# Optimization experiments

Hardware: AMD Instinct MI355X
Metric: run time of the kernel (lower is better)

The kernel has to match this reference:

```python
import jax, jax.numpy as jnp
import numpy as np
import math

N, KZ, IFZ, AHZ, AFZ = 2048, 20, 128, 4, 32
LN_EPS = 1e-5


def setup_inputs() -> dict:
    key = jax.random.key(0)
    ks = jax.random.split(key, 8)
    s = 1.0 / math.sqrt(IFZ)
    return {
        "x_2": jax.random.normal(ks[0], (N, KZ, IFZ), jnp.float32),
        "edge_index": jax.random.randint(ks[1], (N, KZ), 0, N, dtype=jnp.int64),
        "Wq": jax.random.normal(ks[2], (IFZ, AHZ * AFZ), jnp.float32) * s,
        "Wk": jax.random.normal(ks[3], (IFZ, AHZ * AFZ), jnp.float32) * s,
        "Wv": jax.random.normal(ks[4], (IFZ, AHZ * AFZ), jnp.float32) * s,
        "Wb": jax.random.normal(ks[5], (IFZ, AHZ), jnp.float32) * s,
        "Wg": jax.random.normal(ks[6], (IFZ, AHZ * AFZ), jnp.float32) * s,
        "bg": jnp.zeros((AHZ * AFZ,), jnp.float32),
        "Wback": jax.random.normal(ks[7], (AHZ * AFZ, IFZ), jnp.float32) * s,
        "bback": jnp.zeros((IFZ,), jnp.float32),
        "gamma": jnp.ones((IFZ,), jnp.float32),
        "beta": jnp.zeros((IFZ,), jnp.float32),
    }


def _edge_attention(x_2, edge_index, Wq, Wk, Wv, Wb, Wg, bg, Wback, bback, gamma, beta):
    n, kz, _ = x_2.shape
    ahz, afz = AHZ, AFZ
    # projections: [N, kz, ahz, afz]
    q = (x_2 @ Wq).reshape(n, kz, ahz, afz)
    k = (x_2 @ Wk).reshape(n, kz, ahz, afz)
    v = (x_2 @ Wv).reshape(n, kz, ahz, afz)
    gate = jax.nn.sigmoid((x_2 @ Wg + bg).reshape(n, kz, ahz, afz))
    b = x_2 @ Wb  # [N, kz, ahz]
    scale = math.sqrt(afz)
    # neighbor gathers: [N, kz, kz, ahz, afz] (dominant memory traffic)
    k_nb = k[edge_index]
    v_nb = v[edge_index]
    b_nb = b[edge_index]  # [N, kz, kz, ahz]
    # self part: key[edge_temp][n,i,j] == k[n,j] -> avoid materializing broadcast
    s_self = jnp.einsum('nkac,njac->nkja', q, k) / scale + b[:, None, :, :]
    s_nb = jnp.einsum('nkac,nkjac->nkja', q, k_nb) / scale + b_nb
    scores = jnp.concatenate([s_self, s_nb], axis=2)  # [N, kz, 2kz, ahz]
    w = jax.nn.softmax(scores, axis=2)
    w_self, w_nb = w[:, :, :kz], w[:, :, kz:]
    ctx = (jnp.einsum('nkja,njac->nkac', w_self, v)
           + jnp.einsum('nkja,nkjac->nkac', w_nb, v_nb))
    out = gate * ctx  # [N, kz, ahz, afz]
    back = out.reshape(n, kz, ahz * afz) @ Wback + bback
    y = back + math.sqrt(2.0) * x_2
    mu = jnp.mean(y, axis=-1, keepdims=True)
    var = jnp.mean((y - mu) ** 2, axis=-1, keepdims=True)
    return gamma * (y - mu) / jnp.sqrt(var + LN_EPS) + beta


def reference(x_2, edge_index, Wq, Wk, Wv, Wb, Wg, bg, Wback, bback, gamma, beta):
    return _edge_attention(x_2, edge_index, Wq, Wk, Wv, Wb, Wg, bg, Wback, bback, gamma, beta)
```

## Files before the change

kernel.cpp:

```cpp
#include <hip/hip_runtime.h>
#include <math.h>

#define NN   2048
#define KZ   20
#define IFZ  128
#define AHZ  4
#define AFZ  32
#define ROWS (NN*KZ)
#define TWO_KZ (2*KZ)

typedef __attribute__((ext_vector_type(8))) short short8v;
typedef __attribute__((ext_vector_type(4))) float f32x4;
typedef __attribute__((ext_vector_type(2))) float f32x2;

__device__ __forceinline__ float blo(unsigned int u) {
    union { unsigned int i; float f; } x; x.i = u << 16; return x.f;
}
__device__ __forceinline__ float bhi(unsigned int u) {
    union { unsigned int i; float f; } x; x.i = u & 0xffff0000u; return x.f;
}
__device__ __forceinline__ unsigned short f2b(float f) {
    union { float f; unsigned int i; } x; x.f = f;
    unsigned int r = x.i + 0x7fffu + ((x.i >> 16) & 1u);
    return (unsigned short)(r >> 16);
}
__device__ __forceinline__ unsigned pack2(float a, float b) {
    return (unsigned)f2b(a) | ((unsigned)f2b(b) << 16);
}

__global__ __launch_bounds__(256) void setup_kernel(
    const float* __restrict__ x,
    const float* __restrict__ Wq, const float* __restrict__ Wk,
    const float* __restrict__ Wv, const float* __restrict__ Wg,
    const float* __restrict__ Wback, const float* __restrict__ Wb,
    unsigned short* __restrict__ xb, unsigned short* __restrict__ Wt,
    unsigned short* __restrict__ Wbt, float* __restrict__ bbuf)
{
    const int b   = blockIdx.x;
    const int tid = threadIdx.x;

    if (b < 2560) {
        const int gid = b * 256 + tid;
        const float4* src = (const float4*)x;
        float4 v0 = src[gid * 2];
        float4 v1 = src[gid * 2 + 1];
        uint4 o;
        o.x = pack2(v0.x, v0.y);
        o.y = pack2(v0.z, v0.w);
        o.z = pack2(v1.x, v1.y);
        o.w = pack2(v1.z, v1.w);
        ((uint4*)xb)[gid] = o;
    } else if (b < 2880) {
        const int gid = (b - 2560) * 256 + tid;
        if (gid < 512 * 128) {
            const int n = gid >> 7, k = gid & 127;
            const float* W; int c;
            if      (n < 128) { W = Wq; c = n; }
            else if (n < 256) { W = Wk; c = n - 128; }
            else if (n < 384) { W = Wv; c = n - 256; }
            else              { W = Wg; c = n - 384; }
            Wt[gid] = f2b(W[k * 128 + c]);
        } else {
            const int g2 = gid - 512 * 128;
            const int n = g2 >> 7, k = g2 & 127;
            Wbt[g2] = f2b(Wback[k * 128 + n]);
        }
    } else {
        const int row = (b - 2880) * 256 + tid;
        const float4* xv = (const float4*)(x + (size_t)row * IFZ);
        const float4* wv = (const float4*)Wb;
        float4 acc = make_float4(0.f, 0.f, 0.f, 0.f);
        #pragma unroll
        for (int k4 = 0; k4 < 32; ++k4) {
            const float4 xc = xv[k4];
            float4 w;
            w = wv[k4*4+0]; acc.x += xc.x*w.x; acc.y += xc.x*w.y; acc.z += xc.x*w.z; acc.w += xc.x*w.w;
            w = wv[k4*4+1]; acc.x += xc.y*w.x; acc.y += xc.y*w.y; acc.z += xc.y*w.z; acc.w += xc.y*w.w;
            w = wv[k4*4+2]; acc.x += xc.z*w.x; acc.y += xc.z*w.y; acc.z += xc.z*w.z; acc.w += xc.z*w.w;
            w = wv[k4*4+3]; acc.x += xc.w*w.x; acc.y += xc.w*w.y; acc.z += xc.w*w.z; acc.w += xc.w*w.w;
        }
        ((float4*)bbuf)[row] = acc;
    }
}

__global__ __launch_bounds__(256) void proj_gemm(
    const unsigned short* __restrict__ xb, const unsigned short* __restrict__ Wt,
    const float* __restrict__ bg,
    unsigned short* __restrict__ qb, unsigned short* __restrict__ kb,
    unsigned short* __restrict__ gb,
    unsigned char* __restrict__ kf8, unsigned char* __restrict__ vf8)
{
    const int row0 = blockIdx.x * 128;
    const int wid  = threadIdx.x >> 6;
    const int lane = threadIdx.x & 63;
    const int wm = wid >> 1, wn = wid & 1;
    const int l15 = lane & 15, lg = lane >> 4;

    short8v a[4][4];
    {
        const unsigned short* Ab = xb + ((size_t)(row0 + wm*64 + l15)) * IFZ + lg*8;
        #pragma unroll
        for (int ks = 0; ks < 4; ++ks)
            #pragma unroll
            for (int fm = 0; fm < 4; ++fm)
                a[ks][fm] = *((const short8v*)(Ab + (size_t)fm*16*IFZ + ks*32));
    }

    #pragma unroll
    for (int cc = 0; cc < 4; ++cc) {
        const unsigned short* Bb = Wt + ((size_t)(cc*128 + wn*64 + l15)) * IFZ + lg*8;

        f32x4 acc[4][4];
        #pragma unroll
        for (int i = 0; i < 4; ++i)
            #pragma unroll
            for (int j = 0; j < 4; ++j) acc[i][j] = (f32x4){0.f,0.f,0.f,0.f};

        #pragma unroll
        for (int ks = 0; ks < 4; ++ks) {
            short8v b[4];
            #pragma unroll
            for (int f = 0; f < 4; ++f)
                b[f] = *((const short8v*)(Bb + (size_t)f*16*IFZ + ks*32));
            #pragma unroll
            for (int fm = 0; fm < 4; ++fm)
                #pragma unroll
                for (int fn = 0; fn < 4; ++fn)
                    acc[fm][fn] = __builtin_amdgcn_mfma_f32_16x16x32_bf16(
                        b[fn], a[ks][fm], acc[fm][fn], 0, 0, 0);
        }

        const bool gate = (cc == 3);
        unsigned short* ob = (cc == 0) ? qb : (cc == 1) ? kb : (cc == 3) ? gb : (unsigned short*)0;
        unsigned char*  f8 = (cc == 1) ? kf8 : (cc == 2) ? vf8 : (unsigned char*)0;

        #pragma unroll
        for (int fm = 0; fm < 4; ++fm) {
            const int row = row0 + wm*64 + fm*16 + l15;
            #pragma unroll
            for (int fn = 0; fn < 4; ++fn) {
                const int cbase = wn*64 + fn*16 + lg*4;
                float v0 = acc[fm][fn][0], v1 = acc[fm][fn][1];
                float v2 = acc[fm][fn][2], v3 = acc[fm][fn][3];
                if (gate) {
                    const float4 bg4 = *(const float4*)(bg + cbase);
                    v0 = 1.f/(1.f + __expf(-(v0 + bg4.x)));
                    v1 = 1.f/(1.f + __expf(-(v1 + bg4.y)));
                    v2 = 1.f/(1.f + __expf(-(v2 + bg4.z)));
                    v3 = 1.f/(1.f + __expf(-(v3 + bg4.w)));
                }
                if (ob) {
                    uint2 o;
                    o.x = pack2(v0, v1);
                    o.y = pack2(v2, v3);
                    *(uint2*)(ob + (size_t)row * IFZ + cbase) = o;
                }
                if (f8) {
                    int p = __builtin_amdgcn_cvt_pk_fp8_f32(v0, v1, 0, false);
                    p     = __builtin_amdgcn_cvt_pk_fp8_f32(v2, v3, p, true);
                    *(unsigned*)(f8 + (size_t)row*128 + cbase) = (unsigned)p;
                }
            }
        }
    }
}

__global__ __launch_bounds__(256) void attn_back_ln(
    const unsigned short* __restrict__ qb, const unsigned short* __restrict__ kb,
    const unsigned short* __restrict__ gb,
    const float* __restrict__ bbuf, const int* __restrict__ edge,
    const unsigned char* __restrict__ kf8, const unsigned char* __restrict__ vf8,
    const float* __restrict__ x, const unsigned short* __restrict__ Wbt,
    const float* __restrict__ bback, const float* __restrict__ gamma,
    const float* __restrict__ beta, float* __restrict__ out)
{
    const int n   = blockIdx.x;
    const int tid = threadIdx.x;

    __shared__ unsigned qsu[KZ*80];
    __shared__ unsigned ksu[KZ*80];
    __shared__ float    scys[3280];
    __shared__ unsigned ctxb[32*68];
    __shared__ float    bs[KZ*AHZ];
    __shared__ float    st2[KZ][2];
    __shared__ int      es[KZ];

    const size_t base  = (size_t)n * (KZ*IFZ);
    const size_t base2 = base >> 1;

    {
        const uint4* qsrc = (const uint4*)(qb + base);
        const uint4* ksrc = (const uint4*)(kb + base);
        for (int i = tid; i < KZ*16; i += 256) {
            const int r = i >> 4, u4 = i & 15;
            const int d = r*80 + (u4 >> 2)*20 + (u4 & 3)*4;
            *(uint4*)&qsu[d] = qsrc[i];
            *(uint4*)&ksu[d] = ksrc[i];
        }
        for (int i = tid; i < 12*68; i += 256) ctxb[20*68 + i] = 0u;
    }
    if (tid < KZ)      es[tid] = edge[n*KZ + tid];
    if (tid < KZ*AHZ)  bs[tid] = bbuf[(size_t)n*(KZ*AHZ) + tid];
    __syncthreads();

    const float rscale = 0.17677669529663687f;

    if (tid < 240) {
        const int p  = tid / 3, r3 = tid - p*3;
        const int kk = p >> 2, a = p & 3;

        float qf[32];
        {
            const uint4 q0 = *(const uint4*)&qsu[kk*80 + a*20 + 0];
            const uint4 q1 = *(const uint4*)&qsu[kk*80 + a*20 + 4];
            const uint4 q2 = *(const uint4*)&qsu[kk*80 + a*20 + 8];
            const uint4 q3 = *(const uint4*)&qsu[kk*80 + a*20 + 12];
            unsigned qu_[16] = {q0.x,q0.y,q0.z,q0.w, q1.x,q1.y,q1.z,q1.w,
                                q2.x,q2.y,q2.z,q2.w, q3.x,q3.y,q3.z,q3.w};
            #pragma unroll
            for (int c = 0; c < 16; ++c) { qf[2*c] = blo(qu_[c]); qf[2*c+1] = bhi(qu_[c]); }
        }

        for (int j = r3; j < KZ; j += 3) {
            const int kbse = j*80 + a*20;
            const uint4 k0 = *(const uint4*)&ksu[kbse + 0];
            const uint4 k1 = *(const uint4*)&ksu[kbse + 4];
            const uint4 k2 = *(const uint4*)&ksu[kbse + 8];
            const uint4 k3 = *(const uint4*)&ksu[kbse + 12];
            unsigned ku_[16] = {k0.x,k0.y,k0.z,k0.w, k1.x,k1.y,k1.z,k1.w,
                                k2.x,k2.y,k2.z,k2.w, k3.x,k3.y,k3.z,k3.w};
            float s = 0.f;
            #pragma unroll
            for (int c = 0; c < 16; ++c)
                s += qf[2*c]*blo(ku_[c]) + qf[2*c+1]*bhi(ku_[c]);
            scys[p*41 + j] = s*rscale + bs[j*AHZ + a];
        }

        {
            const int e = es[kk];
            for (int jj = r3; jj < KZ; jj += 3) {
                const unsigned char* kp = kf8 + ((size_t)e*KZ + jj)*128 + a*32;
                const uint4 k1 = *(const uint4*)kp;
                const uint4 k2 = *(const uint4*)(kp + 16);
                unsigned ks_[8] = {k1.x, k1.y, k1.z, k1.w, k2.x, k2.y, k2.z, k2.w};
                float s = 0.f;
                #pragma unroll
                for (int u = 0; u < 8; ++u) {
                    const f32x2 lo = __builtin_amdgcn_cvt_pk_f32_fp8(ks_[u], false);
                    const f32x2 hi = __builtin_amdgcn_cvt_pk_f32_fp8(ks_[u], true);
                    s += qf[4*u]*lo.x + qf[4*u+1]*lo.y + qf[4*u+2]*hi.x + qf[4*u+3]*hi.y;
                }
                scys[p*41 + KZ + jj] = s*rscale + bbuf[((size_t)e*KZ + jj)*AHZ + a];
            }
        }
    }
    __syncthreads();

    if (tid < KZ*AHZ) {
        float* row = &scys[tid*41];
        float m = row[0];
        #pragma unroll
        for (int j = 1; j < TWO_KZ; ++j) m = fmaxf(m, row[j]);
        float ssum = 0.f;
        #pragma unroll
        for (int j = 0; j < TWO_KZ; ++j) { const float e = __expf(row[j]-m); row[j] = e; ssum += e; }
        const float inv = 1.f/ssum;
        #pragma unroll
        for (int j = 0; j < TWO_KZ; ++j) row[j] *= inv;
    }
    __syncthreads();

    {
        const int kkg = tid >> 6;
        const int c2  = tid & 63;
        const int a   = c2 >> 4;

        unsigned vs_[KZ];
        {
            const unsigned char* vself = vf8 + (size_t)n*(KZ*128) + c2*2;
            #pragma unroll
            for (int j = 0; j < KZ; ++j)
                vs_[j] = *(const unsigned short*)(vself + j*128);
        }

        const unsigned* gbu = (const unsigned*)gb;

        #pragma unroll
        for (int i = 0; i < 5; ++i) {
            const int kk = kkg*5 + i;
            const float* wrow = &scys[(kk*4 + a)*41];
            float acc0 = 0.f, acc1 = 0.f;
            #pragma unroll
            for (int j = 0; j < KZ; ++j) {
                const f32x2 v2 = __builtin_amdgcn_cvt_pk_f32_fp8(vs_[j], false);
                const float w = wrow[j];
                acc0 += w*v2.x; acc1 += w*v2.y;
            }
            const unsigned char* vnb = vf8 + (size_t)es[kk]*(KZ*128) + c2*2;
            #pragma unroll
            for (int j = 0; j < KZ; ++j) {
                const unsigned u = *(const unsigned short*)(vnb + j*128);
                const f32x2 v2 = __builtin_amdgcn_cvt_pk_f32_fp8(u, false);
                const float w = wrow[KZ + j];
                acc0 += w*v2.x; acc1 += w*v2.y;
            }
            const unsigned gu = gbu[base2 + kk*64 + c2];
            ctxb[kk*68 + c2] = pack2(acc0 * blo(gu), acc1 * bhi(gu));
        }
    }
    __syncthreads();

    const int wid  = tid >> 6;
    const int lane = tid & 63;
    const int l15  = lane & 15, lg = lane >> 4;
    const float SQ2 = 1.4142135623730951f;

    f32x4 bacc[2][2];
    #pragma unroll
    for (int i = 0; i < 2; ++i)
        #pragma unroll
        for (int j = 0; j < 2; ++j) bacc[i][j] = (f32x4){0.f,0.f,0.f,0.f};

    #pragma unroll
    for (int ks = 0; ks < 4; ++ks) {
        short8v bfr[2], afr[2];
        #pragma unroll
        for (int fn = 0; fn < 2; ++fn)
            bfr[fn] = *((const short8v*)(Wbt + (size_t)(wid*32 + fn*16 + l15)*IFZ + ks*32 + lg*8));
        #pragma unroll
        for (int fm = 0; fm < 2; ++fm)
            afr[fm] = *((const short8v*)&ctxb[(fm*16 + l15)*68 + ks*16 + lg*4]);
        #pragma unroll
        for (int fm = 0; fm < 2; ++fm)
            #pragma unroll
            for (int fn = 0; fn < 2; ++fn)
                bacc[fm][fn] = __builtin_amdgcn_mfma_f32_16x16x32_bf16(
                    bfr[fn], afr[fm], bacc[fm][fn], 0, 0, 0);
    }

    for (int i = tid; i < 640; i += 256) {
        const int r = i >> 5, c4 = (i & 31) * 4;
        const float4 xv  = *(const float4*)(x + base + (size_t)r*IFZ + c4);
        const float4 bb4 = *(const float4*)(bback + c4);
        float* yp = &scys[r*132 + c4];
        yp[0] = SQ2*xv.x + bb4.x; yp[1] = SQ2*xv.y + bb4.y;
        yp[2] = SQ2*xv.z + bb4.z; yp[3] = SQ2*xv.w + bb4.w;
    }
    __syncthreads();

    #pragma unroll
    for (int fm = 0; fm < 2; ++fm) {
        const int row = fm*16 + l15;
        if (row < KZ) {
            #pragma unroll
            for (int fn = 0; fn < 2; ++fn) {
                const int cb = wid*32 + fn*16 + lg*4;
                float* yp = &scys[row*132 + cb];
                yp[0] += bacc[fm][fn][0]; yp[1] += bacc[fm][fn][1];
                yp[2] += bacc[fm][fn][2]; yp[3] += bacc[fm][fn][3];
            }
        }
    }
    __syncthreads();

    if (tid < 160) {
        const int row = tid >> 3, t = tid & 7;
        float s1 = 0.f, s2 = 0.f;
        #pragma unroll
        for (int i = 0; i < 16; ++i) {
            const float v = scys[row*132 + t*16 + i];
            s1 += v; s2 += v*v;
        }
        s1 += __shfl_xor(s1, 1); s2 += __shfl_xor(s2, 1);
        s1 += __shfl_xor(s1, 2); s2 += __shfl_xor(s2, 2);
        s1 += __shfl_xor(s1, 4); s2 += __shfl_xor(s2, 4);
        if (t == 0) {
            const float mean = s1 * (1.f/IFZ);
            const float var  = s2 * (1.f/IFZ) - mean*mean;
            st2[row][0] = mean;
            st2[row][1] = rsqrtf(var + 1e-5f);
        }
    }
    __syncthreads();

    for (int i = tid; i < 640; i += 256) {
        const int r = i >> 5, c4 = (i & 31) * 4;
        const float mean = st2[r][0], rstd = st2[r][1];
        const float4 g4 = *(const float4*)(gamma + c4);
        const float4 b4 = *(const float4*)(beta + c4);
        const float4 yv = *(const float4*)&scys[r*132 + c4];
        float4 o;
        o.x = g4.x*(yv.x - mean)*rstd + b4.x;
        o.y = g4.y*(yv.y - mean)*rstd + b4.y;
        o.z = g4.z*(yv.z - mean)*rstd + b4.z;
        o.w = g4.w*(yv.w - mean)*rstd + b4.w;
        *(float4*)(out + base + (size_t)r*IFZ + c4) = o;
    }
}

extern "C" void kernel_launch(void* const* d_in, const int* in_sizes, int n_in,
                              void* d_out, int out_size, void* d_ws, size_t ws_size,
                              hipStream_t stream) {
    const float* x     = (const float*)d_in[0];
    const int*   edge  = (const int*)  d_in[1];
    const float* Wq    = (const float*)d_in[2];
    const float* Wk    = (const float*)d_in[3];
    const float* Wv    = (const float*)d_in[4];
    const float* Wb    = (const float*)d_in[5];
    const float* Wg    = (const float*)d_in[6];
    const float* bg    = (const float*)d_in[7];
    const float* Wback = (const float*)d_in[8];
    const float* bback = (const float*)d_in[9];
    const float* gamma = (const float*)d_in[10];
    const float* beta  = (const float*)d_in[11];
    float* out = (float*)d_out;

    const size_t RE = (size_t)ROWS * IFZ;
    unsigned short* qb  = (unsigned short*)d_ws;
    unsigned short* kb  = qb + RE;
    unsigned short* gb  = kb + RE;
    unsigned short* xb  = gb + RE;
    unsigned short* Wt  = xb + RE;
    unsigned short* Wbt = Wt + 512*128;
    float*          bbuf= (float*)(Wbt + 128*128);
    unsigned char*  kf8 = (unsigned char*)(bbuf + (size_t)ROWS*4);
    unsigned char*  vf8 = kf8 + RE;

    setup_kernel<<<3040, 256, 0, stream>>>(x, Wq, Wk, Wv, Wg, Wback, Wb,
                                           xb, Wt, Wbt, bbuf);
    proj_gemm  <<<ROWS/128, 256, 0, stream>>>(xb, Wt, bg, qb, kb, gb, kf8, vf8);
    attn_back_ln<<<NN, 256, 0, stream>>>(qb, kb, gb, bbuf, edge, kf8, vf8,
                                         x, Wbt, bback, gamma, beta, out);
}
```

Measured before the change: 111.1 us.

## Fuse x bf16 conversion into projection GEMM and alias attention LDS buffers

The separate bf16 conversion pass over x in the setup kernel is removed. The projection GEMM now reads fp32 x directly and packs it to bf16 in registers, which avoids writing and re-reading a bf16 copy of x and shrinks the setup launch. The attention kernel also aliases the context buffer onto the q/k shared-memory region, moving its zero-fill to after those buffers are dead, to cut LDS use and possibly raise occupancy. The cost is that the GEMM loads twice as many bytes for its A operand and does the conversion arithmetic inline.

```diff
diff --git a/kernel.cpp b/kernel.cpp
--- a/kernel.cpp
+++ b/kernel.cpp
@@ -33,25 +33,14 @@
     const float* __restrict__ Wq, const float* __restrict__ Wk,
     const float* __restrict__ Wv, const float* __restrict__ Wg,
     const float* __restrict__ Wback, const float* __restrict__ Wb,
-    unsigned short* __restrict__ xb, unsigned short* __restrict__ Wt,
-    unsigned short* __restrict__ Wbt, float* __restrict__ bbuf)
+    unsigned short* __restrict__ Wt, unsigned short* __restrict__ Wbt,
+    float* __restrict__ bbuf)
 {
     const int b   = blockIdx.x;
     const int tid = threadIdx.x;
 
-    if (b < 2560) {
+    if (b < 320) {
         const int gid = b * 256 + tid;
-        const float4* src = (const float4*)x;
-        float4 v0 = src[gid * 2];
-        float4 v1 = src[gid * 2 + 1];
-        uint4 o;
-        o.x = pack2(v0.x, v0.y);
-        o.y = pack2(v0.z, v0.w);
-        o.z = pack2(v1.x, v1.y);
-        o.w = pack2(v1.z, v1.w);
-        ((uint4*)xb)[gid] = o;
-    } else if (b < 2880) {
-        const int gid = (b - 2560) * 256 + tid;
         if (gid < 512 * 128) {
             const int n = gid >> 7, k = gid & 127;
             const float* W; int c;
@@ -66,7 +55,7 @@
             Wbt[g2] = f2b(Wback[k * 128 + n]);
         }
     } else {
-        const int row = (b - 2880) * 256 + tid;
+        const int row = (b - 320) * 256 + tid;
         const float4* xv = (const float4*)(x + (size_t)row * IFZ);
         const float4* wv = (const float4*)Wb;
         float4 acc = make_float4(0.f, 0.f, 0.f, 0.f);
@@ -84,7 +73,7 @@
 }
 
 __global__ __launch_bounds__(256) void proj_gemm(
-    const unsigned short* __restrict__ xb, const unsigned short* __restrict__ Wt,
+    const float* __restrict__ x, const unsigned short* __restrict__ Wt,
     const float* __restrict__ bg,
     unsigned short* __restrict__ qb, unsigned short* __restrict__ kb,
     unsigned short* __restrict__ gb,
@@ -98,12 +87,20 @@
 
     short8v a[4][4];
     {
-        const unsigned short* Ab = xb + ((size_t)(row0 + wm*64 + l15)) * IFZ + lg*8;
+        const float* Af = x + ((size_t)(row0 + wm*64 + l15)) * IFZ + lg*8;
         #pragma unroll
         for (int ks = 0; ks < 4; ++ks)
             #pragma unroll
-            for (int fm = 0; fm < 4; ++fm)
-                a[ks][fm] = *((const short8v*)(Ab + (size_t)fm*16*IFZ + ks*32));
+            for (int fm = 0; fm < 4; ++fm) {
+                const float4 u0 = *(const float4*)(Af + (size_t)fm*16*IFZ + ks*32);
+                const float4 u1 = *(const float4*)(Af + (size_t)fm*16*IFZ + ks*32 + 4);
+                union { short8v s; uint4 u; } cv;
+                cv.u.x = pack2(u0.x, u0.y);
+                cv.u.y = pack2(u0.z, u0.w);
+                cv.u.z = pack2(u1.x, u1.y);
+                cv.u.w = pack2(u1.z, u1.w);
+                a[ks][fm] = cv.s;
+            }
     }
 
     #pragma unroll
@@ -177,13 +174,15 @@
     const int n   = blockIdx.x;
     const int tid = threadIdx.x;
 
-    __shared__ unsigned qsu[KZ*80];
-    __shared__ unsigned ksu[KZ*80];
+    __shared__ unsigned smemA[KZ*80*2];
     __shared__ float    scys[3280];
-    __shared__ unsigned ctxb[32*68];
     __shared__ float    bs[KZ*AHZ];
     __shared__ float    st2[KZ][2];
     __shared__ int      es[KZ];
+
+    unsigned* qsu  = smemA;
+    unsigned* ksu  = smemA + KZ*80;
+    unsigned* ctxb = smemA;
 
     const size_t base  = (size_t)n * (KZ*IFZ);
     const size_t base2 = base >> 1;
@@ -197,7 +196,6 @@
             *(uint4*)&qsu[d] = qsrc[i];
             *(uint4*)&ksu[d] = ksrc[i];
         }
-        for (int i = tid; i < 12*68; i += 256) ctxb[20*68 + i] = 0u;
     }
     if (tid < KZ)      es[tid] = edge[n*KZ + tid];
     if (tid < KZ*AHZ)  bs[tid] = bbuf[(size_t)n*(KZ*AHZ) + tid];
@@ -271,6 +269,8 @@
     __syncthreads();
 
     {
+        for (int i = tid; i < 12*68; i += 256) ctxb[20*68 + i] = 0u;
+
         const int kkg = tid >> 6;
         const int c2  = tid & 63;
         const int a   = c2 >> 4;
@@ -419,16 +419,15 @@
     unsigned short* qb  = (unsigned short*)d_ws;
     unsigned short* kb  = qb + RE;
     unsigned short* gb  = kb + RE;
-    unsigned short* xb  = gb + RE;
-    unsigned short* Wt  = xb + RE;
+    unsigned short* Wt  = gb + RE;
     unsigned short* Wbt = Wt + 512*128;
     float*          bbuf= (float*)(Wbt + 128*128);
     unsigned char*  kf8 = (unsigned char*)(bbuf + (size_t)ROWS*4);
     unsigned char*  vf8 = kf8 + RE;
 
-    setup_kernel<<<3040, 256, 0, stream>>>(x, Wq, Wk, Wv, Wg, Wback, Wb,
-                                           xb, Wt, Wbt, bbuf);
-    proj_gemm  <<<ROWS/128, 256, 0, stream>>>(xb, Wt, bg, qb, kb, gb, kf8, vf8);
+    setup_kernel<<<480, 256, 0, stream>>>(x, Wq, Wk, Wv, Wg, Wback, Wb,
+                                          Wt, Wbt, bbuf);
+    proj_gemm  <<<ROWS/128, 256, 0, stream>>>(x, Wt, bg, qb, kb, gb, kf8, vf8);
     attn_back_ln<<<NN, 256, 0, stream>>>(qb, kb, gb, bbuf, edge, kf8, vf8,
                                          x, Wbt, bback, gamma, beta, out);
 }
```

After: 106.3 us. 4.3% less time.
